# Kernel optimization log

Hardware: AMD Instinct MI355X
Metric: run time of the kernel (lower is better)

The kernel has to match this reference:

```python
import jax, jax.numpy as jnp
import numpy as np

N = 10000        # num_nodes
F_IN = 256       # dataset_num_features
H = 128          # hidden_channels
C_OUT = 40       # dataset_num_classes
L = 3            # num_layers
HEADS = 8
DH = H // HEADS  # per-head dim
E = 160000       # num edges (before self loops)
SCALE = 1.0 / float(np.sqrt(DH))


def setup_inputs() -> dict:
    key = jax.random.key(0)
    ks = jax.random.split(key, 8)
    s = lambda k, *sh: (jax.random.normal(k, sh, dtype=jnp.float32) * 0.05)
    return dict(
        edge_index=jax.random.randint(ks[0], (2, E), 0, N, dtype=jnp.int32),
        x_param=s(ks[1], N, F_IN),
        lin1_w=s(ks[2], F_IN, H),
        lin1_b=jnp.zeros((H,), jnp.float32),
        wq=s(ks[3], L, H, H),
        wk=s(ks[4], L, H, H),
        wv=s(ks[5], L, H, H),
        bq=jnp.zeros((L, H), jnp.float32),
        bk=jnp.zeros((L, H), jnp.float32),
        bv=jnp.zeros((L, H), jnp.float32),
        lin2_w=s(ks[6], H, C_OUT),
        lin2_b=jnp.zeros((C_OUT,), jnp.float32),
    )


def _gcn_norm(edge_index):
    # PyG gcn_norm: add self loops (weight 1), symmetric D^-1/2 A D^-1/2
    loops = jnp.arange(N, dtype=edge_index.dtype)
    row = jnp.concatenate([edge_index[0], loops])  # source j
    col = jnp.concatenate([edge_index[1], loops])  # target i
    deg = jax.ops.segment_sum(jnp.ones(row.shape, jnp.float32), col, num_segments=N)
    dis = jnp.where(deg > 0, jax.lax.rsqrt(jnp.maximum(deg, 1e-12)), 0.0)
    return row, col, dis[row] * dis[col]


def _restricted_softmax(score):
    # softmax with an implicit extra logit at `margin=0`
    m = jnp.maximum(jnp.max(score, axis=-1, keepdims=True), 0.0)
    e = jnp.exp(score - m)
    return e / (jnp.sum(e, axis=-1, keepdims=True) + jnp.exp(-m))


def _forward(edge_index, x_param, lin1_w, lin1_b, wq, wk, wv, bq, bk, bv, lin2_w, lin2_b):
    row, col, norm = _gcn_norm(edge_index)
    # dropouts are eval-mode no-ops
    x = jax.nn.relu(x_param @ lin1_w + lin1_b)  # [N, H]
    x_all = x[:, None, :]                       # [N, 1, H]
    for l in range(L):
        t = x_all.shape[1]
        # project per-node first (linear commutes with per-edge gather)
        q = (x_all[:, -1] @ wq[l] + bq[l]).reshape(N, HEADS, DH)      # query from latest state
        k = (x_all @ wk[l] + bk[l]).reshape(N, t, HEADS, DH)          # keys over full history
        v = (x_all @ wv[l] + bv[l]).reshape(N, t, HEADS, DH)
        qe = q[col]   # [Etot, heads, dh]   (x_i)
        ke = k[row]   # [Etot, t, heads, dh] (x_j)
        ve = v[row]
        score = jnp.einsum('ehd,ethd->eht', qe, ke) * SCALE
        attn = _restricted_softmax(score)        # attention-dropout is a no-op in eval
        msg = jnp.einsum('eht,ethd->ehd', attn, ve).reshape(-1, H) * norm[:, None]
        out = jax.ops.segment_sum(msg, col, num_segments=N)  # aggr='add'
        x = jax.nn.relu(out)
        x_all = jnp.concatenate([x_all, x[:, None, :]], axis=1)
    logits = x_all[:, -1] @ lin2_w + lin2_b
    return jax.nn.log_softmax(logits, axis=1)


def reference(edge_index, x_param, lin1_w, lin1_b, wq, wk, wv, bq, bk, bv, lin2_w, lin2_b):
    return _forward(edge_index, x_param, lin1_w, lin1_b, wq, wk, wv, bq, bk, bv, lin2_w, lin2_b)
```

## Files before the change

### kernel.cpp

```cpp
#include <hip/hip_runtime.h>
#include <math.h>

#define N_NODES 10000
#define F_IN_D  256
#define H_DIM   128
#define C_OUTD  40
#define NHEADS  8
#define NEDGES  160000
#define ETOT    (NEDGES + N_NODES)
#define SCALE_F 0.25f
#define TILES_N 157
#define KVSZ    ((size_t)N_NODES * 3 * 256)

typedef __attribute__((ext_vector_type(8))) short bf16x8;
typedef __attribute__((ext_vector_type(4))) float f32x4;
typedef __attribute__((ext_vector_type(2))) float f32x2;

__device__ __forceinline__ unsigned short f2bf(float f) {
    unsigned int u = __float_as_uint(f);
    unsigned int r = (u + 0x7FFFu + ((u >> 16) & 1u)) >> 16;
    return (unsigned short)r;
}
__device__ __forceinline__ unsigned char f2fp8(float v) {
    int pk = __builtin_amdgcn_cvt_pk_fp8_f32(v, v, 0, false);
    return (unsigned char)(pk & 0xff);
}


__global__ __launch_bounds__(256) void k_prep_cast(const float* __restrict__ w1,
                                                   const float* __restrict__ wq,
                                                   const float* __restrict__ wk,
                                                   const float* __restrict__ wv,
                                                   const float* __restrict__ w2,
                                                   unsigned short* __restrict__ W1T,
                                                   unsigned short* __restrict__ WTq,
                                                   unsigned short* __restrict__ WTk,
                                                   unsigned short* __restrict__ WTv,
                                                   unsigned short* __restrict__ W2T,
                                                   int* __restrict__ degi) {
    int t = blockIdx.x * 256 + threadIdx.x;
    if (t < 8192) {
        float4 v = *(const float4*)(w1 + 4 * t);
        int e = 4 * t;
        #pragma unroll
        for (int i = 0; i < 4; ++i) {
            int k = (e + i) >> 7, n = (e + i) & 127;
            W1T[n * 256 + k] = f2bf(((const float*)&v)[i]);
        }
    } else if (t < 45056) {
        int u = t - 8192;
        int mat = u >> 12;
        int l = mat / 3, ws = mat % 3;
        const float*    src = (ws == 0) ? wq  : (ws == 1) ? wk  : wv;
        unsigned short* dst = (ws == 0) ? WTq : (ws == 1) ? WTk : WTv;
        int e2 = (u & 4095) * 4;
        float4 v = *(const float4*)(src + l * 16384 + e2);
        #pragma unroll
        for (int i = 0; i < 4; ++i) {
            int k = (e2 + i) >> 7, n = (e2 + i) & 127;
            dst[l * 16384 + n * 128 + k] = f2bf(((const float*)&v)[i]);
        }
    } else if (t < 46336) {
        int e = (t - 45056) * 4;
        float4 v = *(const float4*)(w2 + e);
        #pragma unroll
        for (int i = 0; i < 4; ++i) {
            int ee = e + i;
            int k = ee / 40, c = ee - k * 40;
            W2T[c * 128 + k] = f2bf(((const float*)&v)[i]);
        }
    } else if (t < 46592) {
        int idx = 5120 + (t - 46336) * 4;
        *(uint2*)&W2T[idx] = make_uint2(0u, 0u);
    } else if (t < 49092) {
        int idx = (t - 46592) * 4;
        *(int4*)&degi[idx] = make_int4(0, 0, 0, 0);
    }
}


__device__ __forceinline__ void lin1_block(int bid, int ct0, const float* __restrict__ X,
                                           const unsigned short* __restrict__ W1T,
                                           const float* __restrict__ b1,
                                           unsigned short* __restrict__ X0, int nct) {
    int tid = threadIdx.x;
    int wid = tid >> 6, lane = tid & 63;
    int m = lane & 15, quad = lane >> 4;
    int rowA = bid * 64 + wid * 16 + m;
    int rowc = rowA < N_NODES ? rowA : N_NODES - 1;
    bf16x8 af[8];
    const float* ap = X + (size_t)rowc * F_IN_D + quad * 8;
    #pragma unroll
    for (int s = 0; s < 8; ++s) {
        float4 lo = *(const float4*)(ap + s * 32);
        float4 hi = *(const float4*)(ap + s * 32 + 4);
        union { unsigned short u[8]; bf16x8 v; } pk;
        pk.u[0] = f2bf(lo.x); pk.u[1] = f2bf(lo.y);
        pk.u[2] = f2bf(lo.z); pk.u[3] = f2bf(lo.w);
        pk.u[4] = f2bf(hi.x); pk.u[5] = f2bf(hi.y);
        pk.u[6] = f2bf(hi.z); pk.u[7] = f2bf(hi.w);
        af[s] = pk.v;
    }
    int row0 = bid * 64 + wid * 16 + quad * 4;
    for (int ct = ct0; ct < ct0 + nct; ++ct) {
        int col = ct * 16 + m;
        const unsigned short* bp = W1T + (size_t)col * F_IN_D + quad * 8;
        f32x4 acc = {0.f, 0.f, 0.f, 0.f};
        #pragma unroll
        for (int s = 0; s < 8; ++s) {
            bf16x8 bfr = __builtin_bit_cast(bf16x8, *(const uint4*)(bp + s * 32));
            acc = __builtin_amdgcn_mfma_f32_16x16x32_bf16(af[s], bfr, acc, 0, 0, 0);
        }
        float bb = b1[col];
        #pragma unroll
        for (int rg = 0; rg < 4; ++rg) {
            int r = row0 + rg;
            if (r < N_NODES)
                X0[(size_t)r * H_DIM + col] = f2bf(fmaxf(acc[rg] + bb, 0.f));
        }
    }
}

__device__ __forceinline__ void qkv_block(int mi, int rt,
                                          const unsigned short* __restrict__ XHb,
                                          const unsigned short* __restrict__ WTq_l,
                                          const unsigned short* __restrict__ WTk_l,
                                          const unsigned short* __restrict__ WTv_l,
                                          const float* __restrict__ bq_l,
                                          const float* __restrict__ bk_l,
                                          const float* __restrict__ bv_l,
                                          unsigned short* __restrict__ Qb,
                                          unsigned char* __restrict__ KVb,
                                          int hasQ, int qslice, int nK, int sbase, int nct) {
    int tid = threadIdx.x;
    int wid = tid >> 6, lane = tid & 63;
    int m = lane & 15, quad = lane >> 4;
    const unsigned short* WT; const float* bias; int slice, mode;
    if (hasQ && mi == 0) { WT = WTq_l; bias = bq_l; slice = qslice; mode = 0; }
    else {
        int j = mi - hasQ;
        if (j < nK) { WT = WTk_l; bias = bk_l; slice = sbase + j;      mode = 1; }
        else        { WT = WTv_l; bias = bv_l; slice = sbase + j - nK; mode = 2; }
    }
    const unsigned short* A = XHb + (size_t)slice * N_NODES * H_DIM;
    int rowA = rt * 64 + wid * 16 + m;
    bf16x8 af[4];
    const unsigned short* ap = A + (size_t)rowA * H_DIM + quad * 8;
    #pragma unroll
    for (int s = 0; s < 4; ++s)
        af[s] = __builtin_bit_cast(bf16x8, *(const uint4*)(ap + s * 32));
    int row0 = rt * 64 + wid * 16 + quad * 4;
    int vofs = (mode == 2) ? 8 : 0;
    for (int cp = 0; cp < nct; ++cp) {
        int colA = cp * 32 + m;
        int colB = colA + 16;
        const unsigned short* bpA = WT + (size_t)colA * H_DIM + quad * 8;
        const unsigned short* bpB = WT + (size_t)colB * H_DIM + quad * 8;
        bf16x8 bA[4], bB[4];
        #pragma unroll
        for (int s = 0; s < 4; ++s) {
            bA[s] = __builtin_bit_cast(bf16x8, *(const uint4*)(bpA + s * 32));
            bB[s] = __builtin_bit_cast(bf16x8, *(const uint4*)(bpB + s * 32));
        }
        f32x4 accA = {0.f, 0.f, 0.f, 0.f};
        f32x4 accB = {0.f, 0.f, 0.f, 0.f};
        #pragma unroll
        for (int s = 0; s < 4; ++s) {
            accA = __builtin_amdgcn_mfma_f32_16x16x32_bf16(af[s], bA[s], accA, 0, 0, 0);
            accB = __builtin_amdgcn_mfma_f32_16x16x32_bf16(af[s], bB[s], accB, 0, 0, 0);
        }
        float bbA = bias[colA], bbB = bias[colB];
        #pragma unroll
        for (int rg = 0; rg < 4; ++rg) {
            int r = row0 + rg;
            if (r < N_NODES) {
                float vA = accA[rg] + bbA;
                float vB = accB[rg] + bbB;
                if (mode == 0) {
                    Qb[(size_t)r * H_DIM + colA] = f2bf(vA * SCALE_F);
                    Qb[(size_t)r * H_DIM + colB] = f2bf(vB * SCALE_F);
                } else {
                    size_t nb = ((size_t)r * 3 + slice) * 256;
                    KVb[nb + (colA >> 3) * 16 + (colA & 7) + vofs] = f2fp8(vA);
                    KVb[nb + (colB >> 3) * 16 + (colB & 7) + vofs] = f2fp8(vB);
                }
            }
        }
    }
}


template <int T>
__device__ __forceinline__ void kv_load(const uint4* __restrict__ KV, int r, int ci,
                                        uint4 (&kv)[T]) {
    const uint4* p = KV + (size_t)r * 48 + ci;
    #pragma unroll
    for (int s = 0; s < T; ++s) kv[s] = p[s * 16];
}

template <int T>
__device__ __forceinline__ void edge_accum(const uint4 (&kv)[T], const float (&q)[8],
                                           float nrm, float (&a)[8]) {
    float den = 1.f;
    float mv[8];
    #pragma unroll
    for (int i = 0; i < 8; ++i) mv[i] = 0.f;
    #pragma unroll
    for (int s = 0; s < T; ++s) {
        f32x2 k0 = __builtin_amdgcn_cvt_pk_f32_fp8(kv[s].x, false);
        f32x2 k1 = __builtin_amdgcn_cvt_pk_f32_fp8(kv[s].x, true);
        f32x2 k2 = __builtin_amdgcn_cvt_pk_f32_fp8(kv[s].y, false);
        f32x2 k3 = __builtin_amdgcn_cvt_pk_f32_fp8(kv[s].y, true);
        float p = q[0] * k0[0] + q[1] * k0[1] + q[2] * k1[0] + q[3] * k1[1]
                + q[4] * k2[0] + q[5] * k2[1] + q[6] * k3[0] + q[7] * k3[1];
        p += __shfl_xor(p, 1, 2);
        float w = __expf(p);
        den += w;
        f32x2 v0 = __builtin_amdgcn_cvt_pk_f32_fp8(kv[s].z, false);
        f32x2 v1 = __builtin_amdgcn_cvt_pk_f32_fp8(kv[s].z, true);
        f32x2 v2 = __builtin_amdgcn_cvt_pk_f32_fp8(kv[s].w, false);
        f32x2 v3 = __builtin_amdgcn_cvt_pk_f32_fp8(kv[s].w, true);
        mv[0] += w * v0[0]; mv[1] += w * v0[1];
        mv[2] += w * v1[0]; mv[3] += w * v1[1];
        mv[4] += w * v2[0]; mv[5] += w * v2[1];
        mv[6] += w * v3[0]; mv[7] += w * v3[1];
    }
    float ws = __fdividef(nrm, den);
    #pragma unroll
    for (int i = 0; i < 8; ++i) a[i] += ws * mv[i];
}

template <int T>
__device__ __forceinline__ void attn_block(int bid, const unsigned short* __restrict__ Q,
                                           const uint4* __restrict__ KV,
                                           const int2* __restrict__ csr,
                                           const int* __restrict__ degi,
                                           unsigned int* __restrict__ Xout) {
    int tid = threadIdx.x;
    int wid = tid >> 6, lane = tid & 63;
    int quarter = lane >> 4, ci = lane & 15;
    int n = bid * 4 + wid;

    int cnt = degi[n] + 1;
    if (cnt > 64) cnt = 64;
    int li = lane < cnt ? lane : cnt - 1;
    int2 eAll = csr[(n << 6) + li];
    int   rAll = eAll.x;
    float nAll = (lane < cnt) ? __int_as_float(eAll.y) : 0.f;

    float q[8];
    {
        uint4 qp = *(const uint4*)&Q[(size_t)n * H_DIM + ci * 8];
        q[0] = __uint_as_float(qp.x << 16);
        q[1] = __uint_as_float(qp.x & 0xffff0000u);
        q[2] = __uint_as_float(qp.y << 16);
        q[3] = __uint_as_float(qp.y & 0xffff0000u);
        q[4] = __uint_as_float(qp.z << 16);
        q[5] = __uint_as_float(qp.z & 0xffff0000u);
        q[6] = __uint_as_float(qp.w << 16);
        q[7] = __uint_as_float(qp.w & 0xffff0000u);
    }
    int nq = (cnt + 3) >> 2;
    float a[8];
    #pragma unroll
    for (int i = 0; i < 8; ++i) a[i] = 0.f;

    auto rowN = [&](int j4) { return __shfl(rAll, j4 < 63 ? j4 : 63, 64); };
    auto nrmN = [&](int j4) { return __shfl(nAll, j4 < 63 ? j4 : 63, 64); };

    uint4 kv0[T], kv1[T], kv2[T], kv3[T];
    kv_load<T>(KV, rowN(quarter), ci, kv0);
    kv_load<T>(KV, rowN(4 + quarter), ci, kv1);
    kv_load<T>(KV, rowN(8 + quarter), ci, kv2);
    kv_load<T>(KV, rowN(12 + quarter), ci, kv3);

    int j = 0;
    for (;;) {
        edge_accum<T>(kv0, q, nrmN(j * 4 + quarter), a);
        if (++j >= nq) break;
        kv_load<T>(KV, rowN((j + 3) * 4 + quarter), ci, kv0);
        edge_accum<T>(kv1, q, nrmN(j * 4 + quarter), a);
        if (++j >= nq) break;
        kv_load<T>(KV, rowN((j + 3) * 4 + quarter), ci, kv1);
        edge_accum<T>(kv2, q, nrmN(j * 4 + quarter), a);
        if (++j >= nq) break;
        kv_load<T>(KV, rowN((j + 3) * 4 + quarter), ci, kv2);
        edge_accum<T>(kv3, q, nrmN(j * 4 + quarter), a);
        if (++j >= nq) break;
        kv_load<T>(KV, rowN((j + 3) * 4 + quarter), ci, kv3);
    }

    #pragma unroll
    for (int i = 0; i < 8; ++i) {
        a[i] += __shfl_xor(a[i], 16, 64);
        a[i] += __shfl_xor(a[i], 32, 64);
    }
    if (quarter == 0) {
        uint4 o;
        o.x = ((unsigned int)f2bf(fmaxf(a[1], 0.f)) << 16) | (unsigned int)f2bf(fmaxf(a[0], 0.f));
        o.y = ((unsigned int)f2bf(fmaxf(a[3], 0.f)) << 16) | (unsigned int)f2bf(fmaxf(a[2], 0.f));
        o.z = ((unsigned int)f2bf(fmaxf(a[5], 0.f)) << 16) | (unsigned int)f2bf(fmaxf(a[4], 0.f));
        o.w = ((unsigned int)f2bf(fmaxf(a[7], 0.f)) << 16) | (unsigned int)f2bf(fmaxf(a[6], 0.f));
        *(uint4*)&Xout[(size_t)n * 64 + ci * 4] = o;
    }
}


__global__ __launch_bounds__(256) void k_deg_lin1(const int* __restrict__ col,
                                                  int* __restrict__ degi,
                                                  int* __restrict__ slotbuf,
                                                  const float* __restrict__ X,
                                                  const unsigned short* __restrict__ W1T,
                                                  const float* __restrict__ b1,
                                                  unsigned short* __restrict__ X0, int nct) {
    int b = blockIdx.x;
    if (b < 625) {
        int e = b * 256 + threadIdx.x;
        slotbuf[e] = atomicAdd(&degi[col[e]], 1);
        return;
    }
    int bid = b - 625;
    lin1_block(bid % TILES_N, (bid / TILES_N) * 4, X, W1T, b1, X0, nct);
}

__global__ __launch_bounds__(256) void k_scatter_qkv0(const int* __restrict__ row,
                                                      const int* __restrict__ col,
                                                      const int* __restrict__ degi,
                                                      const int* __restrict__ slotbuf,
                                                      int2* __restrict__ csr,
                                                      const unsigned short* __restrict__ XHb,
                                                      const unsigned short* __restrict__ WTq,
                                                      const unsigned short* __restrict__ WTk,
                                                      const unsigned short* __restrict__ WTv,
                                                      const float* __restrict__ bq,
                                                      const float* __restrict__ bk,
                                                      const float* __restrict__ bv,
                                                      unsigned short* __restrict__ Qb,
                                                      unsigned char* __restrict__ KVb,
                                                      int nct) {
    if (blockIdx.x < 665) {
        int e = blockIdx.x * 256 + threadIdx.x;
        if (e >= ETOT) return;
        int r, c, slot;
        if (e < NEDGES) { r = row[e]; c = col[e]; slot = slotbuf[e]; }
        else            { r = c = e - NEDGES; slot = degi[c]; }
        if (slot > 63) slot = 63;
        float dr = rsqrtf((float)(degi[r] + 1));
        float dc = rsqrtf((float)(degi[c] + 1));
        int2 ent; ent.x = r; ent.y = __float_as_int(dr * dc);
        csr[(c << 6) + slot] = ent;
        return;
    }
    int b = blockIdx.x - 665;
    qkv_block(b / TILES_N, b % TILES_N, XHb, WTq, WTk, WTv, bq, bk, bv,
              Qb, KVb, 1, 0, 1, 0, nct);
}

template <int T>
__global__ __launch_bounds__(256) void k_attn_qkvold(const unsigned short* __restrict__ Q,
                                                     const uint4* __restrict__ KV,
                                                     const int2* __restrict__ csr,
                                                     const int* __restrict__ degi,
                                                     unsigned int* __restrict__ Xout,
                                                     const unsigned short* __restrict__ XHb,
                                                     const unsigned short* __restrict__ WTk_l,
                                                     const unsigned short* __restrict__ WTv_l,
                                                     const float* __restrict__ bk_l,
                                                     const float* __restrict__ bv_l,
                                                     unsigned char* __restrict__ KVnext,
                                                     int nK, int nct) {
    if (blockIdx.x < 2500) {
        attn_block<T>(blockIdx.x, Q, KV, csr, degi, Xout);
        return;
    }
    int b = blockIdx.x - 2500;
    qkv_block(b / TILES_N, b % TILES_N, XHb, nullptr, WTk_l, WTv_l,
              nullptr, bk_l, bv_l, nullptr, KVnext, 0, 0, nK, 0, nct);
}

__global__ __launch_bounds__(256) void k_qkv(const unsigned short* __restrict__ XHb,
                                             const unsigned short* __restrict__ WTq_l,
                                             const unsigned short* __restrict__ WTk_l,
                                             const unsigned short* __restrict__ WTv_l,
                                             const float* __restrict__ bq_l,
                                             const float* __restrict__ bk_l,
                                             const float* __restrict__ bv_l,
                                             unsigned short* __restrict__ Qb,
                                             unsigned char* __restrict__ KVb,
                                             int qslice, int nct) {
    qkv_block(blockIdx.x / TILES_N, blockIdx.x % TILES_N, XHb, WTq_l, WTk_l, WTv_l,
              bq_l, bk_l, bv_l, Qb, KVb, 1, qslice, 1, qslice, nct);
}

template <int T>
__global__ __launch_bounds__(256) void k_attn_agg(const unsigned short* __restrict__ Q,
                                                  const uint4* __restrict__ KV,
                                                  const int2* __restrict__ csr,
                                                  const int* __restrict__ degi,
                                                  unsigned int* __restrict__ Xout) {
    attn_block<T>(blockIdx.x, Q, KV, csr, degi, Xout);
}


__global__ __launch_bounds__(128) void k_lin2_mfma(const unsigned short* __restrict__ X,
                                                   const unsigned short* __restrict__ W2T,
                                                   const float* __restrict__ b2,
                                                   float* __restrict__ out) {
    int tid = threadIdx.x;
    int wid = tid >> 6, lane = tid & 63;
    int m = lane & 15, quad = lane >> 4;
    int rowA = blockIdx.x * 32 + wid * 16 + m;
    bf16x8 af[4];
    const unsigned short* ap = X + (size_t)rowA * H_DIM + quad * 8;
    #pragma unroll
    for (int s = 0; s < 4; ++s)
        af[s] = __builtin_bit_cast(bf16x8, *(const uint4*)(ap + s * 32));

    f32x4 acc0 = {0.f, 0.f, 0.f, 0.f};
    f32x4 acc1 = {0.f, 0.f, 0.f, 0.f};
    f32x4 acc2 = {0.f, 0.f, 0.f, 0.f};
    const unsigned short* bp0 = W2T + (size_t)(m)      * H_DIM + quad * 8;
    const unsigned short* bp1 = W2T + (size_t)(16 + m) * H_DIM + quad * 8;
    const unsigned short* bp2 = W2T + (size_t)(32 + m) * H_DIM + quad * 8;
    #pragma unroll
    for (int s = 0; s < 4; ++s) {
        bf16x8 b0 = __builtin_bit_cast(bf16x8, *(const uint4*)(bp0 + s * 32));
        acc0 = __builtin_amdgcn_mfma_f32_16x16x32_bf16(af[s], b0, acc0, 0, 0, 0);
        bf16x8 b1 = __builtin_bit_cast(bf16x8, *(const uint4*)(bp1 + s * 32));
        acc1 = __builtin_amdgcn_mfma_f32_16x16x32_bf16(af[s], b1, acc1, 0, 0, 0);
        bf16x8 b2f = __builtin_bit_cast(bf16x8, *(const uint4*)(bp2 + s * 32));
        acc2 = __builtin_amdgcn_mfma_f32_16x16x32_bf16(af[s], b2f, acc2, 0, 0, 0);
    }

    float bb0 = b2[m], bb1 = b2[16 + m];
    float bb2 = (m < 8) ? b2[32 + m] : 0.f;
    int row0 = blockIdx.x * 32 + wid * 16 + quad * 4;
    #pragma unroll
    for (int rg = 0; rg < 4; ++rg) {
        int r = row0 + rg;
        float v0 = acc0[rg] + bb0;
        float v1 = acc1[rg] + bb1;
        float v2 = (m < 8) ? (acc2[rg] + bb2) : -INFINITY;
        float mx = fmaxf(fmaxf(v0, v1), v2);
        #pragma unroll
        for (int o = 8; o > 0; o >>= 1) mx = fmaxf(mx, __shfl_xor(mx, o, 16));
        float sm = __expf(v0 - mx) + __expf(v1 - mx) + ((m < 8) ? __expf(v2 - mx) : 0.f);
        #pragma unroll
        for (int o = 8; o > 0; o >>= 1) sm += __shfl_xor(sm, o, 16);
        float lse = mx + __logf(sm);
        if (r < N_NODES) {
            out[(size_t)r * C_OUTD + m]      = v0 - lse;
            out[(size_t)r * C_OUTD + 16 + m] = v1 - lse;
            if (m < 8) out[(size_t)r * C_OUTD + 32 + m] = v2 - lse;
        }
    }
}


extern "C" void kernel_launch(void* const* d_in, const int* in_sizes, int n_in,
                              void* d_out, int out_size, void* d_ws, size_t ws_size,
                              hipStream_t stream) {
    const int*   ei      = (const int*)d_in[0];
    const int*   row     = ei;
    const int*   col     = ei + NEDGES;
    const float* x_param = (const float*)d_in[1];
    const float* lin1_w  = (const float*)d_in[2];
    const float* lin1_b  = (const float*)d_in[3];
    const float* wq      = (const float*)d_in[4];
    const float* wk      = (const float*)d_in[5];
    const float* wv      = (const float*)d_in[6];
    const float* bq      = (const float*)d_in[7];
    const float* bk      = (const float*)d_in[8];
    const float* bv      = (const float*)d_in[9];
    const float* lin2_w  = (const float*)d_in[10];
    const float* lin2_b  = (const float*)d_in[11];
    float*       out     = (float*)d_out;

    char* wbase = (char*)d_ws;
    size_t off = 0;
    auto alloc = [&](size_t bytes) -> void* {
        off = (off + 255) & ~(size_t)255;
        void* p = wbase + off;
        off += bytes;
        return p;
    };
    int*            degi     = (int*)           alloc((size_t)N_NODES * 4);
    int*            slotbuf  = (int*)           alloc((size_t)NEDGES * 4);
    int2*           csr      = (int2*)          alloc((size_t)N_NODES * 64 * 8);
    unsigned short* W1T      = (unsigned short*)alloc((size_t)H_DIM * F_IN_D * 2);
    unsigned short* WTq      = (unsigned short*)alloc((size_t)3 * H_DIM * H_DIM * 2);
    unsigned short* WTk      = (unsigned short*)alloc((size_t)3 * H_DIM * H_DIM * 2);
    unsigned short* WTv      = (unsigned short*)alloc((size_t)3 * H_DIM * H_DIM * 2);
    unsigned short* W2T      = (unsigned short*)alloc((size_t)48 * H_DIM * 2);
    unsigned short* XHb      = (unsigned short*)alloc((size_t)4 * N_NODES * H_DIM * 2);
    unsigned short* Qb       = (unsigned short*)alloc((size_t)N_NODES * H_DIM * 2);
    unsigned char*  KVb      = (unsigned char*) alloc(2 * KVSZ);

    k_prep_cast<<<192, 256, 0, stream>>>(lin1_w, wq, wk, wv, lin2_w,
                                         W1T, WTq, WTk, WTv, W2T, degi);

    k_deg_lin1<<<939, 256, 0, stream>>>(col, degi, slotbuf,
                                        x_param, W1T, lin1_b, XHb, 4);

    k_scatter_qkv0<<<665 + 3 * TILES_N, 256, 0, stream>>>(
        row, col, degi, slotbuf, csr,
        XHb, WTq, WTk, WTv, bq, bk, bv, Qb, KVb, 4);

    unsigned int* X1 = (unsigned int*)(XHb + (size_t)1 * N_NODES * H_DIM);
    unsigned int* X2 = (unsigned int*)(XHb + (size_t)2 * N_NODES * H_DIM);
    unsigned int* X3 = (unsigned int*)(XHb + (size_t)3 * N_NODES * H_DIM);

    k_attn_qkvold<1><<<2500 + 2 * TILES_N, 256, 0, stream>>>(
        Qb, (const uint4*)KVb, csr, degi, X1,
        XHb, WTk + 16384, WTv + 16384, bk + H_DIM, bv + H_DIM,
        KVb + KVSZ, 1, 4);

    k_qkv<<<3 * TILES_N, 256, 0, stream>>>(
        XHb, WTq + 16384, WTk + 16384, WTv + 16384,
        bq + H_DIM, bk + H_DIM, bv + H_DIM, Qb, KVb + KVSZ, 1, 4);

    k_attn_qkvold<2><<<2500 + 4 * TILES_N, 256, 0, stream>>>(
        Qb, (const uint4*)(KVb + KVSZ), csr, degi, X2,
        XHb, WTk + 2 * 16384, WTv + 2 * 16384, bk + 2 * H_DIM, bv + 2 * H_DIM,
        KVb, 2, 4);

    k_qkv<<<3 * TILES_N, 256, 0, stream>>>(
        XHb, WTq + 2 * 16384, WTk + 2 * 16384, WTv + 2 * 16384,
        bq + 2 * H_DIM, bk + 2 * H_DIM, bv + 2 * H_DIM, Qb, KVb, 2, 4);

    k_attn_agg<3><<<2500, 256, 0, stream>>>(Qb, (const uint4*)KVb, csr, degi, X3);

    k_lin2_mfma<<<313, 128, 0, stream>>>(XHb + (size_t)3 * N_NODES * H_DIM,
                                         W2T, lin2_b, out);
}
```

Measured before the change: 219.4 us.

## Fuse lin2+log_softmax into final attention, split QKV column tiles, merge prep

Final-layer attention now computes the lin2 logits and log-softmax directly from its per-node result, so the X3 write, the separate lin2 kernel and one launch go away. The Q/K/V weight casts move into the degree/lin1 kernel, leaving a smaller prep kernel. The QKV projection grids are doubled, with each block handling half the output column tiles, to expose more parallelism. In exchange the logits use scalar dot products with shuffle reductions instead of MFMA, and the doubled grids reload the A tile twice.

```diff
diff --git a/kernel.cpp b/kernel.cpp
--- a/kernel.cpp
+++ b/kernel.cpp
@@ -21,23 +21,18 @@
     unsigned int r = (u + 0x7FFFu + ((u >> 16) & 1u)) >> 16;
     return (unsigned short)r;
 }
+__device__ __forceinline__ float bf2f(unsigned short h) {
+    return __uint_as_float(((unsigned int)h) << 16);
+}
 __device__ __forceinline__ unsigned char f2fp8(float v) {
     int pk = __builtin_amdgcn_cvt_pk_fp8_f32(v, v, 0, false);
     return (unsigned char)(pk & 0xff);
 }
 
 
-__global__ __launch_bounds__(256) void k_prep_cast(const float* __restrict__ w1,
-                                                   const float* __restrict__ wq,
-                                                   const float* __restrict__ wk,
-                                                   const float* __restrict__ wv,
-                                                   const float* __restrict__ w2,
-                                                   unsigned short* __restrict__ W1T,
-                                                   unsigned short* __restrict__ WTq,
-                                                   unsigned short* __restrict__ WTk,
-                                                   unsigned short* __restrict__ WTv,
-                                                   unsigned short* __restrict__ W2T,
-                                                   int* __restrict__ degi) {
+__global__ __launch_bounds__(256) void k_prep1(const float* __restrict__ w1,
+                                               unsigned short* __restrict__ W1T,
+                                               int* __restrict__ degi) {
     int t = blockIdx.x * 256 + threadIdx.x;
     if (t < 8192) {
         float4 v = *(const float4*)(w1 + 4 * t);
@@ -47,33 +42,8 @@
             int k = (e + i) >> 7, n = (e + i) & 127;
             W1T[n * 256 + k] = f2bf(((const float*)&v)[i]);
         }
-    } else if (t < 45056) {
-        int u = t - 8192;
-        int mat = u >> 12;
-        int l = mat / 3, ws = mat % 3;
-        const float*    src = (ws == 0) ? wq  : (ws == 1) ? wk  : wv;
-        unsigned short* dst = (ws == 0) ? WTq : (ws == 1) ? WTk : WTv;
-        int e2 = (u & 4095) * 4;
-        float4 v = *(const float4*)(src + l * 16384 + e2);
-        #pragma unroll
-        for (int i = 0; i < 4; ++i) {
-            int k = (e2 + i) >> 7, n = (e2 + i) & 127;
-            dst[l * 16384 + n * 128 + k] = f2bf(((const float*)&v)[i]);
-        }
-    } else if (t < 46336) {
-        int e = (t - 45056) * 4;
-        float4 v = *(const float4*)(w2 + e);
-        #pragma unroll
-        for (int i = 0; i < 4; ++i) {
-            int ee = e + i;
-            int k = ee / 40, c = ee - k * 40;
-            W2T[c * 128 + k] = f2bf(((const float*)&v)[i]);
-        }
-    } else if (t < 46592) {
-        int idx = 5120 + (t - 46336) * 4;
-        *(uint2*)&W2T[idx] = make_uint2(0u, 0u);
-    } else if (t < 49092) {
-        int idx = (t - 46592) * 4;
+    } else if (t < 10692) {
+        int idx = (t - 8192) * 4;
         *(int4*)&degi[idx] = make_int4(0, 0, 0, 0);
     }
 }
@@ -131,7 +101,8 @@
                                           const float* __restrict__ bv_l,
                                           unsigned short* __restrict__ Qb,
                                           unsigned char* __restrict__ KVb,
-                                          int hasQ, int qslice, int nK, int sbase, int nct) {
+                                          int hasQ, int qslice, int nK, int sbase,
+                                          int cp0, int nct) {
     int tid = threadIdx.x;
     int wid = tid >> 6, lane = tid & 63;
     int m = lane & 15, quad = lane >> 4;
@@ -151,7 +122,7 @@
         af[s] = __builtin_bit_cast(bf16x8, *(const uint4*)(ap + s * 32));
     int row0 = rt * 64 + wid * 16 + quad * 4;
     int vofs = (mode == 2) ? 8 : 0;
-    for (int cp = 0; cp < nct; ++cp) {
+    for (int cp = cp0; cp < cp0 + nct; ++cp) {
         int colA = cp * 32 + m;
         int colB = colA + 16;
         const unsigned short* bpA = WT + (size_t)colA * H_DIM + quad * 8;
@@ -230,12 +201,15 @@
     for (int i = 0; i < 8; ++i) a[i] += ws * mv[i];
 }
 
-template <int T>
+template <int T, bool LOGITS>
 __device__ __forceinline__ void attn_block(int bid, const unsigned short* __restrict__ Q,
                                            const uint4* __restrict__ KV,
                                            const int2* __restrict__ csr,
                                            const int* __restrict__ degi,
-                                           unsigned int* __restrict__ Xout) {
+                                           unsigned int* __restrict__ Xout,
+                                           const unsigned short* __restrict__ W2T,
+                                           const float* __restrict__ b2,
+                                           float* __restrict__ out) {
     int tid = threadIdx.x;
     int wid = tid >> 6, lane = tid & 63;
     int quarter = lane >> 4, ci = lane & 15;
@@ -295,13 +269,54 @@
         a[i] += __shfl_xor(a[i], 16, 64);
         a[i] += __shfl_xor(a[i], 32, 64);
     }
-    if (quarter == 0) {
-        uint4 o;
-        o.x = ((unsigned int)f2bf(fmaxf(a[1], 0.f)) << 16) | (unsigned int)f2bf(fmaxf(a[0], 0.f));
-        o.y = ((unsigned int)f2bf(fmaxf(a[3], 0.f)) << 16) | (unsigned int)f2bf(fmaxf(a[2], 0.f));
-        o.z = ((unsigned int)f2bf(fmaxf(a[5], 0.f)) << 16) | (unsigned int)f2bf(fmaxf(a[4], 0.f));
-        o.w = ((unsigned int)f2bf(fmaxf(a[7], 0.f)) << 16) | (unsigned int)f2bf(fmaxf(a[6], 0.f));
-        *(uint4*)&Xout[(size_t)n * 64 + ci * 4] = o;
+
+    if (!LOGITS) {
+        if (quarter == 0) {
+            uint4 o;
+            o.x = ((unsigned int)f2bf(fmaxf(a[1], 0.f)) << 16) | (unsigned int)f2bf(fmaxf(a[0], 0.f));
+            o.y = ((unsigned int)f2bf(fmaxf(a[3], 0.f)) << 16) | (unsigned int)f2bf(fmaxf(a[2], 0.f));
+            o.z = ((unsigned int)f2bf(fmaxf(a[5], 0.f)) << 16) | (unsigned int)f2bf(fmaxf(a[4], 0.f));
+            o.w = ((unsigned int)f2bf(fmaxf(a[7], 0.f)) << 16) | (unsigned int)f2bf(fmaxf(a[6], 0.f));
+            *(uint4*)&Xout[(size_t)n * 64 + ci * 4] = o;
+        }
+        return;
+    }
+
+    float x[8];
+    #pragma unroll
+    for (int i = 0; i < 8; ++i) x[i] = fmaxf(a[i], 0.f);
+    float lg[10];
+    #pragma unroll
+    for (int jj = 0; jj < 10; ++jj) {
+        int c = quarter * 10 + jj;
+        uint4 w = *(const uint4*)&W2T[c * H_DIM + ci * 8];
+        float p = x[0] * bf2f((unsigned short)(w.x & 0xffff))
+                + x[1] * bf2f((unsigned short)(w.x >> 16))
+                + x[2] * bf2f((unsigned short)(w.y & 0xffff))
+                + x[3] * bf2f((unsigned short)(w.y >> 16))
+                + x[4] * bf2f((unsigned short)(w.z & 0xffff))
+                + x[5] * bf2f((unsigned short)(w.z >> 16))
+                + x[6] * bf2f((unsigned short)(w.w & 0xffff))
+                + x[7] * bf2f((unsigned short)(w.w >> 16));
+        #pragma unroll
+        for (int o = 1; o < 16; o <<= 1) p += __shfl_xor(p, o, 16);
+        lg[jj] = p + b2[c];
+    }
+    float mx = lg[0];
+    #pragma unroll
+    for (int jj = 1; jj < 10; ++jj) mx = fmaxf(mx, lg[jj]);
+    mx = fmaxf(mx, __shfl_xor(mx, 16, 64));
+    mx = fmaxf(mx, __shfl_xor(mx, 32, 64));
+    float sm = 0.f;
+    #pragma unroll
+    for (int jj = 0; jj < 10; ++jj) sm += __expf(lg[jj] - mx);
+    sm += __shfl_xor(sm, 16, 64);
+    sm += __shfl_xor(sm, 32, 64);
+    float lse = mx + __logf(sm);
+    if (ci == 0) {
+        float* op = out + (size_t)n * C_OUTD + quarter * 10;
+        #pragma unroll
+        for (int jj = 0; jj < 10; ++jj) op[jj] = lg[jj] - lse;
     }
 }
 
@@ -312,15 +327,50 @@
                                                   const float* __restrict__ X,
                                                   const unsigned short* __restrict__ W1T,
                                                   const float* __restrict__ b1,
-                                                  unsigned short* __restrict__ X0, int nct) {
+                                                  unsigned short* __restrict__ X0,
+                                                  const float* __restrict__ wq,
+                                                  const float* __restrict__ wk,
+                                                  const float* __restrict__ wv,
+                                                  const float* __restrict__ w2,
+                                                  unsigned short* __restrict__ WTq,
+                                                  unsigned short* __restrict__ WTk,
+                                                  unsigned short* __restrict__ WTv,
+                                                  unsigned short* __restrict__ W2T,
+                                                  int nct) {
     int b = blockIdx.x;
     if (b < 625) {
         int e = b * 256 + threadIdx.x;
         slotbuf[e] = atomicAdd(&degi[col[e]], 1);
         return;
     }
-    int bid = b - 625;
-    lin1_block(bid % TILES_N, (bid / TILES_N) * 4, X, W1T, b1, X0, nct);
+    if (b < 939) {
+        int bid = b - 625;
+        lin1_block(bid % TILES_N, (bid / TILES_N) * 4, X, W1T, b1, X0, nct);
+        return;
+    }
+    int t = (b - 939) * 256 + threadIdx.x;
+    if (t < 36864) {
+        int mat = t >> 12;
+        int l = mat / 3, ws = mat % 3;
+        const float*    src = (ws == 0) ? wq  : (ws == 1) ? wk  : wv;
+        unsigned short* dst = (ws == 0) ? WTq : (ws == 1) ? WTk : WTv;
+        int e2 = (t & 4095) * 4;
+        float4 v = *(const float4*)(src + l * 16384 + e2);
+        #pragma unroll
+        for (int i = 0; i < 4; ++i) {
+            int k = (e2 + i) >> 7, n = (e2 + i) & 127;
+            dst[l * 16384 + n * 128 + k] = f2bf(((const float*)&v)[i]);
+        }
+    } else if (t < 38144) {
+        int e = (t - 36864) * 4;
+        float4 v = *(const float4*)(w2 + e);
+        #pragma unroll
+        for (int i = 0; i < 4; ++i) {
+            int ee = e + i;
+            int k = ee / 40, c = ee - k * 40;
+            W2T[c * H_DIM + k] = f2bf(((const float*)&v)[i]);
+        }
+    }
 }
 
 __global__ __launch_bounds__(256) void k_scatter_qkv0(const int* __restrict__ row,
@@ -336,8 +386,7 @@
                                                       const float* __restrict__ bk,
                                                       const float* __restrict__ bv,
                                                       unsigned short* __restrict__ Qb,
-                                                      unsigned char* __restrict__ KVb,
-                                                      int nct) {
+                                                      unsigned char* __restrict__ KVb) {
     if (blockIdx.x < 665) {
         int e = blockIdx.x * 256 + threadIdx.x;
         if (e >= ETOT) return;
@@ -352,8 +401,10 @@
         return;
     }
     int b = blockIdx.x - 665;
-    qkv_block(b / TILES_N, b % TILES_N, XHb, WTq, WTk, WTv, bq, bk, bv,
-              Qb, KVb, 1, 0, 1, 0, nct);
+    int half = b / (3 * TILES_N);
+    int bb = b % (3 * TILES_N);
+    qkv_block(bb / TILES_N, bb % TILES_N, XHb, WTq, WTk, WTv, bq, bk, bv,
+              Qb, KVb, 1, 0, 1, 0, half * 2, 2);
 }
 
 template <int T>
@@ -368,14 +419,15 @@
                                                      const float* __restrict__ bk_l,
                                                      const float* __restrict__ bv_l,
                                                      unsigned char* __restrict__ KVnext,
-                                                     int nK, int nct) {
+                                                     int nK) {
     if (blockIdx.x < 2500) {
-        attn_block<T>(blockIdx.x, Q, KV, csr, degi, Xout);
+        attn_block<T, false>(blockIdx.x, Q, KV, csr, degi, Xout,
+                             nullptr, nullptr, nullptr);
         return;
     }
     int b = blockIdx.x - 2500;
     qkv_block(b / TILES_N, b % TILES_N, XHb, nullptr, WTk_l, WTv_l,
-              nullptr, bk_l, bv_l, nullptr, KVnext, 0, 0, nK, 0, nct);
+              nullptr, bk_l, bv_l, nullptr, KVnext, 0, 0, nK, 0, 0, 4);
 }
 
 __global__ __launch_bounds__(256) void k_qkv(const unsigned short* __restrict__ XHb,
@@ -387,73 +439,21 @@
                                              const float* __restrict__ bv_l,
                                              unsigned short* __restrict__ Qb,
                                              unsigned char* __restrict__ KVb,
-                                             int qslice, int nct) {
-    qkv_block(blockIdx.x / TILES_N, blockIdx.x % TILES_N, XHb, WTq_l, WTk_l, WTv_l,
-              bq_l, bk_l, bv_l, Qb, KVb, 1, qslice, 1, qslice, nct);
-}
-
-template <int T>
-__global__ __launch_bounds__(256) void k_attn_agg(const unsigned short* __restrict__ Q,
-                                                  const uint4* __restrict__ KV,
-                                                  const int2* __restrict__ csr,
-                                                  const int* __restrict__ degi,
-                                                  unsigned int* __restrict__ Xout) {
-    attn_block<T>(blockIdx.x, Q, KV, csr, degi, Xout);
-}
-
-
-__global__ __launch_bounds__(128) void k_lin2_mfma(const unsigned short* __restrict__ X,
-                                                   const unsigned short* __restrict__ W2T,
-                                                   const float* __restrict__ b2,
-                                                   float* __restrict__ out) {
-    int tid = threadIdx.x;
-    int wid = tid >> 6, lane = tid & 63;
-    int m = lane & 15, quad = lane >> 4;
-    int rowA = blockIdx.x * 32 + wid * 16 + m;
-    bf16x8 af[4];
-    const unsigned short* ap = X + (size_t)rowA * H_DIM + quad * 8;
-    #pragma unroll
-    for (int s = 0; s < 4; ++s)
-        af[s] = __builtin_bit_cast(bf16x8, *(const uint4*)(ap + s * 32));
-
-    f32x4 acc0 = {0.f, 0.f, 0.f, 0.f};
-    f32x4 acc1 = {0.f, 0.f, 0.f, 0.f};
-    f32x4 acc2 = {0.f, 0.f, 0.f, 0.f};
-    const unsigned short* bp0 = W2T + (size_t)(m)      * H_DIM + quad * 8;
-    const unsigned short* bp1 = W2T + (size_t)(16 + m) * H_DIM + quad * 8;
-    const unsigned short* bp2 = W2T + (size_t)(32 + m) * H_DIM + quad * 8;
-    #pragma unroll
-    for (int s = 0; s < 4; ++s) {
-        bf16x8 b0 = __builtin_bit_cast(bf16x8, *(const uint4*)(bp0 + s * 32));
-        acc0 = __builtin_amdgcn_mfma_f32_16x16x32_bf16(af[s], b0, acc0, 0, 0, 0);
-        bf16x8 b1 = __builtin_bit_cast(bf16x8, *(const uint4*)(bp1 + s * 32));
-        acc1 = __builtin_amdgcn_mfma_f32_16x16x32_bf16(af[s], b1, acc1, 0, 0, 0);
-        bf16x8 b2f = __builtin_bit_cast(bf16x8, *(const uint4*)(bp2 + s * 32));
-        acc2 = __builtin_amdgcn_mfma_f32_16x16x32_bf16(af[s], b2f, acc2, 0, 0, 0);
-    }
-
-    float bb0 = b2[m], bb1 = b2[16 + m];
-    float bb2 = (m < 8) ? b2[32 + m] : 0.f;
-    int row0 = blockIdx.x * 32 + wid * 16 + quad * 4;
-    #pragma unroll
-    for (int rg = 0; rg < 4; ++rg) {
-        int r = row0 + rg;
-        float v0 = acc0[rg] + bb0;
-        float v1 = acc1[rg] + bb1;
-        float v2 = (m < 8) ? (acc2[rg] + bb2) : -INFINITY;
-        float mx = fmaxf(fmaxf(v0, v1), v2);
-        #pragma unroll
-        for (int o = 8; o > 0; o >>= 1) mx = fmaxf(mx, __shfl_xor(mx, o, 16));
-        float sm = __expf(v0 - mx) + __expf(v1 - mx) + ((m < 8) ? __expf(v2 - mx) : 0.f);
-        #pragma unroll
-        for (int o = 8; o > 0; o >>= 1) sm += __shfl_xor(sm, o, 16);
-        float lse = mx + __logf(sm);
-        if (r < N_NODES) {
-            out[(size_t)r * C_OUTD + m]      = v0 - lse;
-            out[(size_t)r * C_OUTD + 16 + m] = v1 - lse;
-            if (m < 8) out[(size_t)r * C_OUTD + 32 + m] = v2 - lse;
-        }
-    }
+                                             int qslice) {
+    int half = blockIdx.x / (3 * TILES_N);
+    int bb = blockIdx.x % (3 * TILES_N);
+    qkv_block(bb / TILES_N, bb % TILES_N, XHb, WTq_l, WTk_l, WTv_l,
+              bq_l, bk_l, bv_l, Qb, KVb, 1, qslice, 1, qslice, half * 2, 2);
+}
+
+__global__ __launch_bounds__(256) void k_attn_logits(const unsigned short* __restrict__ Q,
+                                                     const uint4* __restrict__ KV,
+                                                     const int2* __restrict__ csr,
+                                                     const int* __restrict__ degi,
+                                                     const unsigned short* __restrict__ W2T,
+                                                     const float* __restrict__ b2,
+                                                     float* __restrict__ out) {
+    attn_block<3, true>(blockIdx.x, Q, KV, csr, degi, nullptr, W2T, b2, out);
 }
 
 
@@ -491,45 +491,43 @@
     unsigned short* WTq      = (unsigned short*)alloc((size_t)3 * H_DIM * H_DIM * 2);
     unsigned short* WTk      = (unsigned short*)alloc((size_t)3 * H_DIM * H_DIM * 2);
     unsigned short* WTv      = (unsigned short*)alloc((size_t)3 * H_DIM * H_DIM * 2);
-    unsigned short* W2T      = (unsigned short*)alloc((size_t)48 * H_DIM * 2);
-    unsigned short* XHb      = (unsigned short*)alloc((size_t)4 * N_NODES * H_DIM * 2);
+    unsigned short* W2T      = (unsigned short*)alloc((size_t)C_OUTD * H_DIM * 2);
+    unsigned short* XHb      = (unsigned short*)alloc((size_t)3 * N_NODES * H_DIM * 2);
     unsigned short* Qb       = (unsigned short*)alloc((size_t)N_NODES * H_DIM * 2);
     unsigned char*  KVb      = (unsigned char*) alloc(2 * KVSZ);
 
-    k_prep_cast<<<192, 256, 0, stream>>>(lin1_w, wq, wk, wv, lin2_w,
-                                         W1T, WTq, WTk, WTv, W2T, degi);
-
-    k_deg_lin1<<<939, 256, 0, stream>>>(col, degi, slotbuf,
-                                        x_param, W1T, lin1_b, XHb, 4);
-
-    k_scatter_qkv0<<<665 + 3 * TILES_N, 256, 0, stream>>>(
+    k_prep1<<<42, 256, 0, stream>>>(lin1_w, W1T, degi);
+
+    k_deg_lin1<<<1089, 256, 0, stream>>>(col, degi, slotbuf,
+                                         x_param, W1T, lin1_b, XHb,
+                                         wq, wk, wv, lin2_w,
+                                         WTq, WTk, WTv, W2T, 4);
+
+    k_scatter_qkv0<<<665 + 6 * TILES_N, 256, 0, stream>>>(
         row, col, degi, slotbuf, csr,
-        XHb, WTq, WTk, WTv, bq, bk, bv, Qb, KVb, 4);
+        XHb, WTq, WTk, WTv, bq, bk, bv, Qb, KVb);
 
     unsigned int* X1 = (unsigned int*)(XHb + (size_t)1 * N_NODES * H_DIM);
     unsigned int* X2 = (unsigned int*)(XHb + (size_t)2 * N_NODES * H_DIM);
-    unsigned int* X3 = (unsigned int*)(XHb + (size_t)3 * N_NODES * H_DIM);
 
     k_attn_qkvold<1><<<2500 + 2 * TILES_N, 256, 0, stream>>>(
         Qb, (const uint4*)KVb, csr, degi, X1,
         XHb, WTk + 16384, WTv + 16384, bk + H_DIM, bv + H_DIM,
-        KVb + KVSZ, 1, 4);
-
-    k_qkv<<<3 * TILES_N, 256, 0, stream>>>(
+        KVb + KVSZ, 1);
+
+    k_qkv<<<6 * TILES_N, 256, 0, stream>>>(
         XHb, WTq + 16384, WTk + 16384, WTv + 16384,
-        bq + H_DIM, bk + H_DIM, bv + H_DIM, Qb, KVb + KVSZ, 1, 4);
+        bq + H_DIM, bk + H_DIM, bv + H_DIM, Qb, KVb + KVSZ, 1);
 
     k_attn_qkvold<2><<<2500 + 4 * TILES_N, 256, 0, stream>>>(
         Qb, (const uint4*)(KVb + KVSZ), csr, degi, X2,
         XHb, WTk + 2 * 16384, WTv + 2 * 16384, bk + 2 * H_DIM, bv + 2 * H_DIM,
-        KVb, 2, 4);
-
-    k_qkv<<<3 * TILES_N, 256, 0, stream>>>(
+        KVb, 2);
+
+    k_qkv<<<6 * TILES_N, 256, 0, stream>>>(
         XHb, WTq + 2 * 16384, WTk + 2 * 16384, WTv + 2 * 16384,
-        bq + 2 * H_DIM, bk + 2 * H_DIM, bv + 2 * H_DIM, Qb, KVb, 2, 4);
-
-    k_attn_agg<3><<<2500, 256, 0, stream>>>(Qb, (const uint4*)KVb, csr, degi, X3);
-
-    k_lin2_mfma<<<313, 128, 0, stream>>>(XHb + (size_t)3 * N_NODES * H_DIM,
-                                         W2T, lin2_b, out);
-}
+        bq + 2 * H_DIM, bk + 2 * H_DIM, bv + 2 * H_DIM, Qb, KVb, 2);
+
+    k_attn_logits<<<2500, 256, 0, stream>>>(Qb, (const uint4*)KVb, csr, degi,
+                                            W2T, lin2_b, out);
+}
```

After: 217.1 us. About the same (-1.1%).
